# Kernel optimization log

Measured on AMD Instinct MI355X. Metric: run time of the kernel, lower is better.

Reference implementation:

```python
import jax, jax.numpy as jnp
import numpy as np

EPS = 1e-12  # matches torch F.normalize default eps

def setup_inputs() -> dict:
    key = jax.random.key(0)
    k1, k2, k3, k4 = jax.random.split(key, 4)
    B, C, H, W = 4, 256, 32, 32
    D, K = 2048, 16384
    return {
        "hidden_states": jax.random.normal(k1, (B, C, H, W), dtype=jnp.float32),
        "codebook": jax.random.normal(k2, (K, D), dtype=jnp.float32),
        "qc_w": jax.random.normal(k3, (D, C), dtype=jnp.float32) * 0.02,
        "qc_b": jax.random.normal(k4, (D,), dtype=jnp.float32) * 0.02,
    }

def _l2norm(x):
    # F.normalize(p=2, dim=-1): x / max(||x||, eps)
    n = jnp.sqrt(jnp.sum(x * x, axis=-1, keepdims=True))
    return x / jnp.maximum(n, EPS)

def reference(hidden_states, codebook, qc_w, qc_b):
    B, C, H, W = hidden_states.shape
    D = qc_w.shape[0]
    # quant_conv: 1x1 conv == per-pixel linear projection C -> D
    h = jnp.einsum("bchw,dc->bdhw", hidden_states, qc_w) + qc_b[None, :, None, None]
    # flatten to tokens: (B*H*W, D)
    flat = h.transpose(0, 2, 3, 1).reshape(-1, D)
    hn = _l2norm(flat)                  # (N, D)
    en = _l2norm(codebook)              # (K, D)
    sim = hn @ en.T                     # (N, K) cosine similarity
    idx = jnp.argmax(sim, axis=1)       # (N,)
    quant = en[idx]                     # gather normalized codes
    quant = quant.reshape(B, H, W, D).transpose(0, 3, 1, 2)
    return quant, idx
```

## Files before the change

kernel.cpp:

```cpp
#include <hip/hip_runtime.h>
#include <hip/hip_fp16.h>
#include <stdint.h>

#define NTOK 4096
#define KCB  16384
#define CAP  256
#define MAXL 8
#define MARGIN_C 0.02f
#define MARGIN_F 0.02f

typedef _Float16 f16;
typedef _Float16 f16x8 __attribute__((ext_vector_type(8)));
typedef float f32x4 __attribute__((ext_vector_type(4)));
typedef double f64x4 __attribute__((ext_vector_type(4)));

typedef const __attribute__((address_space(1))) uint32_t* gptr_t;
typedef __attribute__((address_space(3))) uint32_t* lptr_t;
__device__ __forceinline__ void gload_lds16(const void* g, void* l) {
  __builtin_amdgcn_global_load_lds((gptr_t)g, (lptr_t)l, 16, 0, 0);
}

__global__ void k_init(int* cnt, int* bad) {
  int i = blockIdx.x * 256 + threadIdx.x;
  if (i < NTOK) cnt[i] = 0;
  if (blockIdx.x == 0 && threadIdx.x == 0) *bad = 0;
}

__global__ __launch_bounds__(256) void k_build_wT(const float* qc_w, const float* qc_b, f16* wT) {
  __shared__ float tl[64][65];
  int d0 = blockIdx.x * 64, c0 = blockIdx.y * 64;
  int jj = threadIdx.x & 63, i0 = threadIdx.x >> 6;
  for (int ii = 0; ii < 64; ii += 4) {
    int i = ii + i0; int d = d0 + i; int c = c0 + jj;
    float v = 0.f;
    if (c < 256) v = qc_w[(size_t)d * 256 + c];
    else if (c == 256) v = qc_b[d];
    tl[i][jj] = v;
  }
  __syncthreads();
  for (int jj2 = 0; jj2 < 64; jj2 += 4) {
    int j = jj2 + i0; int i = threadIdx.x & 63;
    wT[(size_t)(c0 + j) * 2048 + d0 + i] = (f16)tl[i][j];
  }
}

__global__ __launch_bounds__(256) void k_build_x(const float* hid, f16* x16, float* x32) {
  __shared__ float tl[64][65];
  int hw0 = blockIdx.x * 64, c0 = blockIdx.y * 64, b = blockIdx.z;
  int jj = threadIdx.x & 63, i0 = threadIdx.x >> 6;
  for (int ii = 0; ii < 64; ii += 4) {
    int i = ii + i0;
    tl[i][jj] = hid[((size_t)b * 256 + c0 + i) * 1024 + hw0 + jj];
  }
  __syncthreads();
  for (int jj2 = 0; jj2 < 64; jj2 += 4) {
    int j = jj2 + i0; int i = threadIdx.x & 63;
    int t = b * 1024 + hw0 + j; float v = tl[i][j];
    x32[(size_t)t * 256 + c0 + i] = v;
    x16[(size_t)t * 320 + c0 + i] = (f16)v;
  }
  if (blockIdx.y == 0) {
    int tb = b * 1024 + hw0;
    for (int q = 0; q < 16; q++) {
      int idx2 = threadIdx.x * 16 + q;
      int tl2 = idx2 >> 6, p = idx2 & 63;
      x16[(size_t)(tb + tl2) * 320 + 256 + p] = (p == 0) ? (f16)1.0f : (f16)0.0f;
    }
  }
}

__global__ __launch_bounds__(256) void k_proj_mfma(const float* x32, const float* qc_w, const float* qc_b,
                                                   double* h64, int* bad) {
  __shared__ double At[32][66];
  __shared__ double Bt[32][130];
  int d0 = blockIdx.x * 128, t0 = blockIdx.y * 64;
  int tid = threadIdx.x, wid = tid >> 6, lane = tid & 63;
  int cl = lane & 15, g = lane >> 4;

  double ta1 = (double)cl;
  double tb1 = (g == 0) ? 1.0 : 0.0;
  f64x4 tc1 = {0.0, 0.0, 0.0, 0.0};
  tc1 = __builtin_amdgcn_mfma_f64_16x16x4f64(ta1, tb1, tc1, 0, 0, 0);
  double ta2 = (g == 0) ? 1.0 : 0.0;
  double tb2 = (g == 0) ? (double)cl : 0.0;
  f64x4 tc2 = {0.0, 0.0, 0.0, 0.0};
  tc2 = __builtin_amdgcn_mfma_f64_16x16x4f64(ta2, tb2, tc2, 0, 0, 0);
  bool std_ok = true, alt_ok = true, col_ok = true;
#pragma unroll
  for (int r = 0; r < 4; r++) {
    std_ok = std_ok && (tc1[r] == (double)(4 * g + r));
    alt_ok = alt_ok && (tc1[r] == (double)(g + 4 * r));
    col_ok = col_ok && (tc2[r] == (double)cl);
  }
  unsigned long long mstd = __ballot(std_ok), malt = __ballot(alt_ok), mcol = __ballot(col_ok);
  bool all_std = (mstd == ~0ull), all_alt = (malt == ~0ull), all_col = (mcol == ~0ull);
  bool good = (all_std || all_alt) && all_col;
  if (!good) { if (tid == 0) atomicOr(bad, 1); return; }
  int use_alt = all_alt ? 1 : 0;

  int t_a = tid & 63, ka = (tid >> 6) * 8;
  int d_b = tid & 127, kb = (tid >> 7) * 16;
  f32x4 ra0, ra1, rb0, rb1, rb2, rb3;
  auto ldregs = [&](int kc) {
    ra0 = *(const f32x4*)(x32 + (size_t)(t0 + t_a) * 256 + kc + ka);
    ra1 = *(const f32x4*)(x32 + (size_t)(t0 + t_a) * 256 + kc + ka + 4);
    rb0 = *(const f32x4*)(qc_w + (size_t)(d0 + d_b) * 256 + kc + kb);
    rb1 = *(const f32x4*)(qc_w + (size_t)(d0 + d_b) * 256 + kc + kb + 4);
    rb2 = *(const f32x4*)(qc_w + (size_t)(d0 + d_b) * 256 + kc + kb + 8);
    rb3 = *(const f32x4*)(qc_w + (size_t)(d0 + d_b) * 256 + kc + kb + 12);
  };
  ldregs(0);

  f64x4 acc[4][2];
#pragma unroll
  for (int i = 0; i < 4; i++)
#pragma unroll
    for (int j = 0; j < 2; j++) acc[i][j] = (f64x4)0.0;

  for (int c = 0; c < 8; c++) {
    __syncthreads();
#pragma unroll
    for (int e = 0; e < 4; e++) {
      At[ka + e][t_a] = (double)ra0[e];
      At[ka + 4 + e][t_a] = (double)ra1[e];
      Bt[kb + e][d_b] = (double)rb0[e];
      Bt[kb + 4 + e][d_b] = (double)rb1[e];
      Bt[kb + 8 + e][d_b] = (double)rb2[e];
      Bt[kb + 12 + e][d_b] = (double)rb3[e];
    }
    __syncthreads();
    if (c < 7) ldregs((c + 1) * 32);
#pragma unroll
    for (int k4 = 0; k4 < 8; k4++) {
      int k = k4 * 4 + g;
      double a[4], b[2];
#pragma unroll
      for (int i = 0; i < 4; i++) a[i] = At[k][16 * i + cl];
#pragma unroll
      for (int j = 0; j < 2; j++) b[j] = Bt[k][32 * wid + 16 * j + cl];
#pragma unroll
      for (int i = 0; i < 4; i++)
#pragma unroll
        for (int j = 0; j < 2; j++)
          acc[i][j] = __builtin_amdgcn_mfma_f64_16x16x4f64(a[i], b[j], acc[i][j], 0, 0, 0);
    }
  }
#pragma unroll
  for (int i = 0; i < 4; i++)
#pragma unroll
    for (int j = 0; j < 2; j++) {
      int d = d0 + 32 * wid + 16 * j + cl;
      double bias = (double)qc_b[d];
#pragma unroll
      for (int r = 0; r < 4; r++) {
        int row = use_alt ? (g + 4 * r) : (4 * g + r);
        int t = t0 + 16 * i + row;
        h64[(size_t)t * 2048 + d] = acc[i][j][r] + bias;
      }
    }
}

__global__ __launch_bounds__(256) void k_proj_fb(const float* x32, const float* qc_w, const float* qc_b,
                                                 double* h64, const int* bad) {
  if (*bad == 0) return;
  __shared__ double At[16][128];
  __shared__ double Bt[16][16][9];
  int t0 = blockIdx.y * 128, d0 = blockIdx.x * 128;
  int tid = threadIdx.x;
  int tr = tid >> 4, dc = tid & 15;
  int srow = tid & 127, kh = (tid >> 7) * 8;
  int sg = srow >> 3, se = srow & 7;
  const float* pA = x32 + (size_t)(t0 + srow) * 256 + kh;
  const float* pB = qc_w + (size_t)(d0 + srow) * 256 + kh;
  f32x4 a0 = *(const f32x4*)pA, a1 = *(const f32x4*)(pA + 4);
  f32x4 b0 = *(const f32x4*)pB, b1 = *(const f32x4*)(pB + 4);
  double acc[8][8] = {};
  for (int kk = 0; kk < 256; kk += 16) {
    __syncthreads();
#pragma unroll
    for (int j = 0; j < 4; j++) {
      At[kh + j][srow] = (double)a0[j]; At[kh + 4 + j][srow] = (double)a1[j];
      Bt[kh + j][sg][se] = (double)b0[j]; Bt[kh + 4 + j][sg][se] = (double)b1[j];
    }
    __syncthreads();
    if (kk + 16 < 256) {
      a0 = *(const f32x4*)(pA + kk + 16); a1 = *(const f32x4*)(pA + kk + 20);
      b0 = *(const f32x4*)(pB + kk + 16); b1 = *(const f32x4*)(pB + kk + 20);
    }
#pragma unroll
    for (int k = 0; k < 16; k++) {
      double a[8], b[8];
#pragma unroll
      for (int j = 0; j < 8; j++) a[j] = At[k][tr * 8 + j];
#pragma unroll
      for (int j = 0; j < 8; j++) b[j] = Bt[k][dc][j];
#pragma unroll
      for (int i = 0; i < 8; i++)
#pragma unroll
        for (int j = 0; j < 8; j++)
          acc[i][j] = fma(a[i], b[j], acc[i][j]);
    }
  }
#pragma unroll
  for (int i = 0; i < 8; i++)
#pragma unroll
    for (int j = 0; j < 8; j++) {
      int col = d0 + dc * 8 + j;
      h64[(size_t)(t0 + tr * 8 + i) * 2048 + col] = acc[i][j] + (double)qc_b[col];
    }
}

__global__ __launch_bounds__(256) void k_pgemm4(const float* cb, const f16* wT, f16* P16kt,
                                                double* inv64, float* inv32) {
  __shared__ f16 Al[2][64][32];
  __shared__ f16 Bl[2][160][32];
  __shared__ double nsum[64][4];
  __shared__ double invsh[64];
  int j0 = blockIdx.x * 64;
  int c0 = blockIdx.y * 160;
  int tid = threadIdx.x, wid = tid >> 6, lane = tid & 63;
  int cl = lane & 15, g = lane >> 4;
  f32x4 acc[10];
#pragma unroll
  for (int n = 0; n < 10; n++) acc[n] = (f32x4)0.0f;
  int arow = tid & 63, aseg = tid >> 6;
  double s2 = 0.0;

  auto aload = [&](int kk, f32x4& v0, f32x4& v1) {
    v0 = *(const f32x4*)(cb + (size_t)(j0 + arow) * 2048 + kk + aseg * 8);
    v1 = *(const f32x4*)(cb + (size_t)(j0 + arow) * 2048 + kk + aseg * 8 + 4);
  };
  auto addnorm = [&](f32x4 v0, f32x4 v1) {
#pragma unroll
    for (int e = 0; e < 4; e++) {
      s2 += (double)v0[e] * (double)v0[e];
      s2 += (double)v1[e] * (double)v1[e];
    }
  };
  auto awrite = [&](int buf, f32x4 v0, f32x4 v1) {
    f16x8 h;
#pragma unroll
    for (int e = 0; e < 4; e++) { h[e] = (f16)v0[e]; h[4 + e] = (f16)v1[e]; }
    int sp = aseg ^ ((arow >> 1) & 3);
    *(f16x8*)((char*)&Al[buf][arow][0] + sp * 16) = h;
  };
  auto stageB = [&](int kk, int buf) {
#pragma unroll
    for (int i = 0; i < 3; i++) {
      int g2 = wid + 4 * i;
      if (g2 < 10) {
        int r0 = 16 * g2;
        int rl = r0 + (lane >> 2);
        int sl = (lane & 3) ^ ((rl >> 1) & 3);
        gload_lds16(wT + (size_t)(c0 + rl) * 2048 + kk + sl * 8, &Bl[buf][r0][0]);
      }
    }
  };
  auto rdA = [&](int buf, int r, int sg2) -> f16x8 {
    return *(const f16x8*)((const char*)&Al[buf][0][0] + r * 64 + ((sg2 ^ ((r >> 1) & 3)) << 4));
  };
  auto rdB = [&](int buf, int r, int sg2) -> f16x8 {
    return *(const f16x8*)((const char*)&Bl[buf][0][0] + r * 64 + ((sg2 ^ ((r >> 1) & 3)) << 4));
  };

  { f32x4 v0, v1; aload(0, v0, v1); addnorm(v0, v1); awrite(0, v0, v1); }
  stageB(0, 0);
  asm volatile("s_waitcnt vmcnt(0)" ::: "memory");
  __syncthreads();
  for (int s = 0; s < 64; s++) {
    int buf = s & 1;
    f32x4 v0, v1;
    if (s < 63) { aload((s + 1) * 32, v0, v1); stageB((s + 1) * 32, buf ^ 1); }
    f16x8 av = rdA(buf, 16 * wid + cl, g);
#pragma unroll
    for (int n = 0; n < 10; n++) {
      f16x8 bv = rdB(buf, 16 * n + cl, g);
      acc[n] = __builtin_amdgcn_mfma_f32_16x16x32_f16(av, bv, acc[n], 0, 0, 0);
    }
    if (s < 63) { addnorm(v0, v1); awrite(buf ^ 1, v0, v1); }
    asm volatile("s_waitcnt vmcnt(0)" ::: "memory");
    __syncthreads();
  }
  nsum[arow][aseg] = s2;
  __syncthreads();
  if (tid < 64) {
    double t = nsum[tid][0] + nsum[tid][1] + nsum[tid][2] + nsum[tid][3];
    double nn = sqrt(t); nn = fmax(nn, 1e-12);
    double iv = 1.0 / nn;
    invsh[tid] = iv;
    if (blockIdx.y == 0) { inv64[j0 + tid] = iv; inv32[j0 + tid] = (float)iv; }
  }
  __syncthreads();
#pragma unroll
  for (int r = 0; r < 4; r++) {
    int rloc = 16 * wid + 4 * g + r;
    int row = j0 + rloc;
    float sc = (float)invsh[rloc];
#pragma unroll
    for (int n = 0; n < 10; n++) {
      int c = c0 + 16 * n + cl;
      int ks = c >> 5;
      int sl = ((c & 31) >> 3) ^ ((row >> 1) & 3);
      P16kt[(((size_t)ks * KCB + row) << 5) + (sl << 3) + (c & 7)] = (f16)(acc[n][r] * sc);
    }
  }
}

__global__ __launch_bounds__(512) void k_screen14(const f16* x16, const f16* P16kt,
                                                  int* cnt, float* cand_v, int* cand_i) {
  __shared__ f16 Al[2][256][32];
  __shared__ f16 Bl[2][256][32];
  __shared__ float smx[256][4];
  int bid = blockIdx.x;
  int nb = ((bid & 7) << 3) | ((bid >> 3) & 7);
  int tb = bid >> 6;
  int n0 = nb * 256, t0 = tb * 256;
  int tid = threadIdx.x, wid = tid >> 6, lane = tid & 63;
  int wr = wid >> 2, wc = wid & 3;
  int cl = lane & 15, g = lane >> 4;
  f32x4 acc[8][4];
#pragma unroll
  for (int m = 0; m < 8; m++)
#pragma unroll
    for (int n = 0; n < 4; n++) acc[m][n] = (f32x4)0.0f;

  auto stageA = [&](int ks, int buf) {
#pragma unroll
    for (int i = 0; i < 2; i++) {
      int r0 = 32 * wid + 16 * i;
      int rl = r0 + (lane >> 2);
      int sl = (lane & 3) ^ ((rl >> 1) & 3);
      gload_lds16(x16 + (size_t)(t0 + rl) * 320 + ks * 32 + sl * 8, &Al[buf][r0][0]);
    }
  };
  auto stageB = [&](int ks, int buf) {
    const f16* src = P16kt + (((size_t)ks * KCB + n0) << 5) + wid * 1024 + lane * 8;
    gload_lds16(src, &Bl[buf][wid * 32][0]);
    gload_lds16(src + 512, &Bl[buf][wid * 32 + 16][0]);
  };
  auto rdA = [&](int buf, int r, int sg) -> f16x8 {
    return *(const f16x8*)((const char*)&Al[buf][0][0] + r * 64 + ((sg ^ ((r >> 1) & 3)) << 4));
  };
  auto rdB = [&](int buf, int r, int sg) -> f16x8 {
    return *(const f16x8*)((const char*)&Bl[buf][0][0] + r * 64 + ((sg ^ ((r >> 1) & 3)) << 4));
  };

  stageA(0, 0); stageB(0, 0);
  __syncthreads();
#pragma unroll
  for (int s = 0; s < 10; s++) {
    const int buf = s & 1;
    if (s < 9) { stageA(s + 1, buf ^ 1); stageB(s + 1, buf ^ 1); }
    f16x8 av[8], bv[4];
#pragma unroll
    for (int m = 0; m < 8; m++) av[m] = rdA(buf, 128 * wr + 16 * m + cl, g);
#pragma unroll
    for (int n = 0; n < 4; n++) bv[n] = rdB(buf, 64 * wc + 16 * n + cl, g);
    __builtin_amdgcn_s_setprio(1);
#pragma unroll
    for (int m = 0; m < 8; m++)
#pragma unroll
      for (int n = 0; n < 4; n++)
        acc[m][n] = __builtin_amdgcn_mfma_f32_16x16x32_f16(av[m], bv[n], acc[m][n], 0, 0, 0);
    __builtin_amdgcn_s_setprio(0);
    __syncthreads();
  }

#pragma unroll
  for (int m = 0; m < 8; m++) {
#pragma unroll
    for (int r = 0; r < 4; r++) {
      float v = -3.4e38f;
#pragma unroll
      for (int n = 0; n < 4; n++) v = fmaxf(v, acc[m][n][r]);
      v = fmaxf(v, __shfl_xor(v, 1));
      v = fmaxf(v, __shfl_xor(v, 2));
      v = fmaxf(v, __shfl_xor(v, 4));
      v = fmaxf(v, __shfl_xor(v, 8));
      if (cl == 0) smx[128 * wr + 16 * m + 4 * g + r][wc] = v;
    }
  }
  __syncthreads();

  uint32_t* lcnt = (uint32_t*)(&Al[0][0][0]);
  float*    lval = (float*)(lcnt + 256);
  int*      lidx = (int*)(lval + 256 * MAXL);
  if (tid < 256) lcnt[tid] = 0;
  __syncthreads();

#pragma unroll
  for (int m = 0; m < 8; m++) {
#pragma unroll
    for (int r = 0; r < 4; r++) {
      int rloc = 128 * wr + 16 * m + 4 * g + r;
      float lim = fmaxf(fmaxf(smx[rloc][0], smx[rloc][1]), fmaxf(smx[rloc][2], smx[rloc][3])) - MARGIN_C;
#pragma unroll
      for (int n = 0; n < 4; n++) {
        float vv = acc[m][n][r];
        if (vv >= lim) {
          uint32_t p = atomicAdd(&lcnt[rloc], 1u);
          int code = n0 + 64 * wc + 16 * n + cl;
          if (p < MAXL) { lval[rloc * MAXL + p] = vv; lidx[rloc * MAXL + p] = code; }
          else {
            int slot = atomicAdd(&cnt[t0 + rloc], 1);
            if (slot < CAP) { cand_v[(t0 + rloc) * CAP + slot] = vv; cand_i[(t0 + rloc) * CAP + slot] = code; }
          }
        }
      }
    }
  }
  __syncthreads();

  if (tid < 256) {
    int lc = (int)lcnt[tid]; if (lc > MAXL) lc = MAXL;
    if (lc > 0) {
      int row = t0 + tid;
      int base = atomicAdd(&cnt[row], lc);
      for (int i = 0; i < lc; i++) {
        int slot = base + i;
        if (slot < CAP) {
          cand_v[row * CAP + slot] = lval[tid * MAXL + i];
          cand_i[row * CAP + slot] = lidx[tid * MAXL + i];
        }
      }
    }
  }
}

__global__ __launch_bounds__(64) void k_rescore3(const double* h64, const float* cb, const double* inv64,
                                                 const int* cnt, const float* cand_v, const int* cand_i,
                                                 float* idxf, int* idxi) {
  int t = blockIdx.x;
  int lane = threadIdx.x;
  int ctot = cnt[t];
  double bV = -1e300; int bI = 0x7fffffff;
  const double* hrow = h64 + (size_t)t * 2048;
  if (ctot <= CAP) {
    float gm = -3.4e38f;
    for (int c = lane; c < ctot; c += 64) gm = fmaxf(gm, cand_v[t * CAP + c]);
#pragma unroll
    for (int o = 32; o; o >>= 1) gm = fmaxf(gm, __shfl_xor(gm, o));
    float lim = gm - MARGIN_F;
    for (int c = 0; c < ctot; c++) {
      float v = cand_v[t * CAP + c];
      if (v < lim) continue;
      int code = cand_i[t * CAP + c];
      const float* crow = cb + (size_t)code * 2048;
      double p = 0.0;
#pragma unroll
      for (int e = 0; e < 32; e++) {
        int d = lane + 64 * e;
        p = fma(hrow[d], (double)crow[d], p);
      }
#pragma unroll
      for (int o = 32; o; o >>= 1) p += __shfl_xor(p, o);
      double sv = p * inv64[code];
      if (sv > bV || (sv == bV && code < bI)) { bV = sv; bI = code; }
    }
  } else {
    for (int code = 0; code < KCB; code++) {
      const float* crow = cb + (size_t)code * 2048;
      double p = 0.0;
      for (int e = 0; e < 32; e++) {
        int d = lane + 64 * e;
        p = fma(hrow[d], (double)crow[d], p);
      }
      for (int o = 32; o; o >>= 1) p += __shfl_xor(p, o);
      double sv = p * inv64[code];
      if (sv > bV || (sv == bV && code < bI)) { bV = sv; bI = code; }
    }
  }
  if (lane == 0) { idxi[t] = bI; idxf[t] = (float)bI; }
}

__global__ __launch_bounds__(256) void k_quant(const float* cb, const float* inv32, const int* idxi, float* out0) {
  int hw = blockIdx.x * 256 + threadIdx.x;
  int d = blockIdx.y, b = blockIdx.z;
  int t = b * 1024 + hw;
  int row = idxi[t];
  out0[((size_t)b * 2048 + d) * 1024 + hw] = cb[(size_t)row * 2048 + d] * inv32[row];
}

extern "C" void kernel_launch(void* const* d_in, const int* in_sizes, int n_in,
                              void* d_out, int out_size, void* d_ws, size_t ws_size,
                              hipStream_t stream) {
  const float* hid = (const float*)d_in[0];
  const float* cb  = (const float*)d_in[1];
  const float* qw  = (const float*)d_in[2];
  const float* qb  = (const float*)d_in[3];
  float* out = (float*)d_out;

  char* w = (char*)d_ws;
  size_t off = 0;
  auto alloc = [&](size_t bytes) -> void* {
    void* p = w + off;
    off += (bytes + 255) & ~(size_t)255;
    return p;
  };
  double* h64   = (double*)alloc((size_t)NTOK * 2048 * 8);
  f16*    x16   = (f16*)   alloc((size_t)NTOK * 320 * 2);
  float*  x32   = (float*) alloc((size_t)NTOK * 256 * 4);
  f16*    wT    = (f16*)   alloc((size_t)320 * 2048 * 2);
  f16*    P16kt = (f16*)   alloc((size_t)10 * KCB * 32 * 2);
  double* inv64 = (double*)alloc((size_t)KCB * 8);
  float*  inv32 = (float*) alloc((size_t)KCB * 4);
  int*    cnt   = (int*)   alloc((size_t)NTOK * 4);
  float*  cand_v= (float*) alloc((size_t)NTOK * CAP * 4);
  int*    cand_i= (int*)   alloc((size_t)NTOK * CAP * 4);
  int*    idxi  = (int*)   alloc((size_t)NTOK * 4);
  int*    bad   = (int*)   alloc(256);

  k_init<<<16, 256, 0, stream>>>(cnt, bad);
  k_build_wT<<<dim3(32, 5), 256, 0, stream>>>(qw, qb, wT);
  k_build_x<<<dim3(16, 4, 4), 256, 0, stream>>>(hid, x16, x32);
  k_proj_mfma<<<dim3(16, 64), 256, 0, stream>>>(x32, qw, qb, h64, bad);
  k_proj_fb<<<dim3(16, 32), 256, 0, stream>>>(x32, qw, qb, h64, bad);
  k_pgemm4<<<dim3(256, 2), 256, 0, stream>>>(cb, wT, P16kt, inv64, inv32);
  k_screen14<<<1024, 512, 0, stream>>>(x16, P16kt, cnt, cand_v, cand_i);
  k_rescore3<<<NTOK, 64, 0, stream>>>(h64, cb, inv64, cnt, cand_v, cand_i, out + 8388608, idxi);
  k_quant<<<dim3(4, 2048, 4), 256, 0, stream>>>(cb, inv32, idxi, out);
}
```

Measured before the change: 359.4 us.

## Fuse fp64 projection into screening kernel via interleaved block roles

Merges the fp64 MFMA projection (h64) and the fp16 screening GEMM into a single launch. Every third block computes a 128x128 projection tile while the other blocks do screening, all sharing one shared-memory buffer. The goal is to overlap the FP64-bound projection with the FP16 screening and drop a kernel launch, since the two are independent. The projection blocks now use 512 threads with a larger tile, and the fused kernel carries the larger shared-memory footprint, which may reduce occupancy for the screening blocks.

Result: no change. 355.8 us (-1.0%).

```diff
diff --git a/kernel.cpp b/kernel.cpp
--- a/kernel.cpp
+++ b/kernel.cpp
@@ -67,97 +67,6 @@
       x16[(size_t)(tb + tl2) * 320 + 256 + p] = (p == 0) ? (f16)1.0f : (f16)0.0f;
     }
   }
-}
-
-__global__ __launch_bounds__(256) void k_proj_mfma(const float* x32, const float* qc_w, const float* qc_b,
-                                                   double* h64, int* bad) {
-  __shared__ double At[32][66];
-  __shared__ double Bt[32][130];
-  int d0 = blockIdx.x * 128, t0 = blockIdx.y * 64;
-  int tid = threadIdx.x, wid = tid >> 6, lane = tid & 63;
-  int cl = lane & 15, g = lane >> 4;
-
-  double ta1 = (double)cl;
-  double tb1 = (g == 0) ? 1.0 : 0.0;
-  f64x4 tc1 = {0.0, 0.0, 0.0, 0.0};
-  tc1 = __builtin_amdgcn_mfma_f64_16x16x4f64(ta1, tb1, tc1, 0, 0, 0);
-  double ta2 = (g == 0) ? 1.0 : 0.0;
-  double tb2 = (g == 0) ? (double)cl : 0.0;
-  f64x4 tc2 = {0.0, 0.0, 0.0, 0.0};
-  tc2 = __builtin_amdgcn_mfma_f64_16x16x4f64(ta2, tb2, tc2, 0, 0, 0);
-  bool std_ok = true, alt_ok = true, col_ok = true;
-#pragma unroll
-  for (int r = 0; r < 4; r++) {
-    std_ok = std_ok && (tc1[r] == (double)(4 * g + r));
-    alt_ok = alt_ok && (tc1[r] == (double)(g + 4 * r));
-    col_ok = col_ok && (tc2[r] == (double)cl);
-  }
-  unsigned long long mstd = __ballot(std_ok), malt = __ballot(alt_ok), mcol = __ballot(col_ok);
-  bool all_std = (mstd == ~0ull), all_alt = (malt == ~0ull), all_col = (mcol == ~0ull);
-  bool good = (all_std || all_alt) && all_col;
-  if (!good) { if (tid == 0) atomicOr(bad, 1); return; }
-  int use_alt = all_alt ? 1 : 0;
-
-  int t_a = tid & 63, ka = (tid >> 6) * 8;
-  int d_b = tid & 127, kb = (tid >> 7) * 16;
-  f32x4 ra0, ra1, rb0, rb1, rb2, rb3;
-  auto ldregs = [&](int kc) {
-    ra0 = *(const f32x4*)(x32 + (size_t)(t0 + t_a) * 256 + kc + ka);
-    ra1 = *(const f32x4*)(x32 + (size_t)(t0 + t_a) * 256 + kc + ka + 4);
-    rb0 = *(const f32x4*)(qc_w + (size_t)(d0 + d_b) * 256 + kc + kb);
-    rb1 = *(const f32x4*)(qc_w + (size_t)(d0 + d_b) * 256 + kc + kb + 4);
-    rb2 = *(const f32x4*)(qc_w + (size_t)(d0 + d_b) * 256 + kc + kb + 8);
-    rb3 = *(const f32x4*)(qc_w + (size_t)(d0 + d_b) * 256 + kc + kb + 12);
-  };
-  ldregs(0);
-
-  f64x4 acc[4][2];
-#pragma unroll
-  for (int i = 0; i < 4; i++)
-#pragma unroll
-    for (int j = 0; j < 2; j++) acc[i][j] = (f64x4)0.0;
-
-  for (int c = 0; c < 8; c++) {
-    __syncthreads();
-#pragma unroll
-    for (int e = 0; e < 4; e++) {
-      At[ka + e][t_a] = (double)ra0[e];
-      At[ka + 4 + e][t_a] = (double)ra1[e];
-      Bt[kb + e][d_b] = (double)rb0[e];
-      Bt[kb + 4 + e][d_b] = (double)rb1[e];
-      Bt[kb + 8 + e][d_b] = (double)rb2[e];
-      Bt[kb + 12 + e][d_b] = (double)rb3[e];
-    }
-    __syncthreads();
-    if (c < 7) ldregs((c + 1) * 32);
-#pragma unroll
-    for (int k4 = 0; k4 < 8; k4++) {
-      int k = k4 * 4 + g;
-      double a[4], b[2];
-#pragma unroll
-      for (int i = 0; i < 4; i++) a[i] = At[k][16 * i + cl];
-#pragma unroll
-      for (int j = 0; j < 2; j++) b[j] = Bt[k][32 * wid + 16 * j + cl];
-#pragma unroll
-      for (int i = 0; i < 4; i++)
-#pragma unroll
-        for (int j = 0; j < 2; j++)
-          acc[i][j] = __builtin_amdgcn_mfma_f64_16x16x4f64(a[i], b[j], acc[i][j], 0, 0, 0);
-    }
-  }
-#pragma unroll
-  for (int i = 0; i < 4; i++)
-#pragma unroll
-    for (int j = 0; j < 2; j++) {
-      int d = d0 + 32 * wid + 16 * j + cl;
-      double bias = (double)qc_b[d];
-#pragma unroll
-      for (int r = 0; r < 4; r++) {
-        int row = use_alt ? (g + 4 * r) : (4 * g + r);
-        int t = t0 + 16 * i + row;
-        h64[(size_t)t * 2048 + d] = acc[i][j][r] + bias;
-      }
-    }
 }
 
 __global__ __launch_bounds__(256) void k_proj_fb(const float* x32, const float* qc_w, const float* qc_b,
@@ -306,18 +215,115 @@
   }
 }
 
-__global__ __launch_bounds__(512) void k_screen14(const f16* x16, const f16* P16kt,
-                                                  int* cnt, float* cand_v, int* cand_i) {
-  __shared__ f16 Al[2][256][32];
-  __shared__ f16 Bl[2][256][32];
-  __shared__ float smx[256][4];
+__global__ __launch_bounds__(512) void k_fused(const f16* x16, const f16* P16kt,
+                                               const float* x32, const float* qc_w, const float* qc_b,
+                                               double* h64, int* bad,
+                                               int* cnt, float* cand_v, int* cand_i) {
+  __shared__ __align__(16) char smem[69632];
   int bid = blockIdx.x;
-  int nb = ((bid & 7) << 3) | ((bid >> 3) & 7);
-  int tb = bid >> 6;
+  int tid = threadIdx.x, lane = tid & 63;
+  int cl = lane & 15, g = lane >> 4;
+  int rr3 = bid % 3;
+
+  if (rr3 == 2) {
+    int pb = bid / 3;
+    int d0 = (pb & 15) * 128, t0 = (pb >> 4) * 128;
+    int half = tid >> 8, htid = tid & 255;
+    int hwid = htid >> 6;
+    int t0h = t0 + half * 64;
+
+    double ta1 = (double)cl;
+    double tb1 = (g == 0) ? 1.0 : 0.0;
+    f64x4 tc1 = {0.0, 0.0, 0.0, 0.0};
+    tc1 = __builtin_amdgcn_mfma_f64_16x16x4f64(ta1, tb1, tc1, 0, 0, 0);
+    double ta2 = (g == 0) ? 1.0 : 0.0;
+    double tb2 = (g == 0) ? (double)cl : 0.0;
+    f64x4 tc2 = {0.0, 0.0, 0.0, 0.0};
+    tc2 = __builtin_amdgcn_mfma_f64_16x16x4f64(ta2, tb2, tc2, 0, 0, 0);
+    bool std_ok = true, alt_ok = true, col_ok = true;
+#pragma unroll
+    for (int r = 0; r < 4; r++) {
+      std_ok = std_ok && (tc1[r] == (double)(4 * g + r));
+      alt_ok = alt_ok && (tc1[r] == (double)(g + 4 * r));
+      col_ok = col_ok && (tc2[r] == (double)cl);
+    }
+    unsigned long long mstd = __ballot(std_ok), malt = __ballot(alt_ok), mcol = __ballot(col_ok);
+    bool all_std = (mstd == ~0ull), all_alt = (malt == ~0ull), all_col = (mcol == ~0ull);
+    bool good = (all_std || all_alt) && all_col;
+    if (!good) { if (tid == 0) atomicOr(bad, 1); return; }
+    int use_alt = all_alt ? 1 : 0;
+
+    double (*At)[32][66] = (double(*)[32][66])smem;
+    double (*Bt)[130] = (double(*)[130])(smem + 33792);
+
+    int t_a = htid & 63, ka = (htid >> 6) * 8;
+    int d_b = tid & 127, kb = (tid >> 7) * 8;
+    f32x4 ra0, ra1, rb0, rb1;
+    auto ldregs = [&](int kc) {
+      ra0 = *(const f32x4*)(x32 + (size_t)(t0h + t_a) * 256 + kc + ka);
+      ra1 = *(const f32x4*)(x32 + (size_t)(t0h + t_a) * 256 + kc + ka + 4);
+      rb0 = *(const f32x4*)(qc_w + (size_t)(d0 + d_b) * 256 + kc + kb);
+      rb1 = *(const f32x4*)(qc_w + (size_t)(d0 + d_b) * 256 + kc + kb + 4);
+    };
+    ldregs(0);
+
+    f64x4 acc[4][2];
+#pragma unroll
+    for (int i = 0; i < 4; i++)
+#pragma unroll
+      for (int j = 0; j < 2; j++) acc[i][j] = (f64x4)0.0;
+
+    for (int c = 0; c < 8; c++) {
+      __syncthreads();
+#pragma unroll
+      for (int e = 0; e < 4; e++) {
+        At[half][ka + e][t_a] = (double)ra0[e];
+        At[half][ka + 4 + e][t_a] = (double)ra1[e];
+        Bt[kb + e][d_b] = (double)rb0[e];
+        Bt[kb + 4 + e][d_b] = (double)rb1[e];
+      }
+      __syncthreads();
+      if (c < 7) ldregs((c + 1) * 32);
+#pragma unroll
+      for (int k4 = 0; k4 < 8; k4++) {
+        int k = k4 * 4 + g;
+        double a[4], b[2];
+#pragma unroll
+        for (int i = 0; i < 4; i++) a[i] = At[half][k][16 * i + cl];
+#pragma unroll
+        for (int j = 0; j < 2; j++) b[j] = Bt[k][32 * hwid + 16 * j + cl];
+#pragma unroll
+        for (int i = 0; i < 4; i++)
+#pragma unroll
+          for (int j = 0; j < 2; j++)
+            acc[i][j] = __builtin_amdgcn_mfma_f64_16x16x4f64(a[i], b[j], acc[i][j], 0, 0, 0);
+      }
+    }
+#pragma unroll
+    for (int i = 0; i < 4; i++)
+#pragma unroll
+      for (int j = 0; j < 2; j++) {
+        int d = d0 + 32 * hwid + 16 * j + cl;
+        double bias = (double)qc_b[d];
+#pragma unroll
+        for (int r = 0; r < 4; r++) {
+          int row = use_alt ? (g + 4 * r) : (4 * g + r);
+          int t = t0h + 16 * i + row;
+          h64[(size_t)t * 2048 + d] = acc[i][j][r] + bias;
+        }
+      }
+    return;
+  }
+
+  int sb = (bid / 3) * 2 + rr3;
+  f16 (*Al)[256][32] = (f16(*)[256][32])smem;
+  f16 (*Bl)[256][32] = (f16(*)[256][32])(smem + 32768);
+  float (*smx)[4] = (float(*)[4])(smem + 65536);
+  int nb = ((sb & 7) << 3) | ((sb >> 3) & 7);
+  int tb = sb >> 6;
   int n0 = nb * 256, t0 = tb * 256;
-  int tid = threadIdx.x, wid = tid >> 6, lane = tid & 63;
+  int wid = tid >> 6;
   int wr = wid >> 2, wc = wid & 3;
-  int cl = lane & 15, g = lane >> 4;
   f32x4 acc[8][4];
 #pragma unroll
   for (int m = 0; m < 8; m++)
@@ -382,7 +388,7 @@
   }
   __syncthreads();
 
-  uint32_t* lcnt = (uint32_t*)(&Al[0][0][0]);
+  uint32_t* lcnt = (uint32_t*)smem;
   float*    lval = (float*)(lcnt + 256);
   int*      lidx = (int*)(lval + 256 * MAXL);
   if (tid < 256) lcnt[tid] = 0;
@@ -513,10 +519,9 @@
   k_init<<<16, 256, 0, stream>>>(cnt, bad);
   k_build_wT<<<dim3(32, 5), 256, 0, stream>>>(qw, qb, wT);
   k_build_x<<<dim3(16, 4, 4), 256, 0, stream>>>(hid, x16, x32);
-  k_proj_mfma<<<dim3(16, 64), 256, 0, stream>>>(x32, qw, qb, h64, bad);
+  k_pgemm4<<<dim3(256, 2), 256, 0, stream>>>(cb, wT, P16kt, inv64, inv32);
+  k_fused<<<1536, 512, 0, stream>>>(x16, P16kt, x32, qw, qb, h64, bad, cnt, cand_v, cand_i);
   k_proj_fb<<<dim3(16, 32), 256, 0, stream>>>(x32, qw, qb, h64, bad);
-  k_pgemm4<<<dim3(256, 2), 256, 0, stream>>>(cb, wT, P16kt, inv64, inv32);
-  k_screen14<<<1024, 512, 0, stream>>>(x16, P16kt, cnt, cand_v, cand_i);
   k_rescore3<<<NTOK, 64, 0, stream>>>(h64, cb, inv64, cnt, cand_v, cand_i, out + 8388608, idxi);
   k_quant<<<dim3(4, 2048, 4), 256, 0, stream>>>(cb, inv32, idxi, out);
 }
```
